# Kernel tuning notes

Measured on AMD Instinct MI355X. Metric: run time of the kernel, lower is better.

The kernel has to match this reference:

```python
import jax, jax.numpy as jnp
import numpy as np

BINS = 100
ALPHA = 0.1

def entropy_batch(h):
    # Faithful to torch: histogram path is detached (done in numpy in original).
    h = jax.lax.stop_gradient(h)
    B, D = h.shape
    hp = h - jnp.min(h, axis=1, keepdims=True)
    hn = hp / jnp.max(hp, axis=1, keepdims=True)  # normalized to [0, 1]
    # np.histogram with `bins` uniform bins over [0,1]; rightmost edge inclusive -> clip
    idx = jnp.clip(jnp.floor(hn * BINS).astype(jnp.int32), 0, BINS - 1)
    rows = jnp.arange(B)[:, None]
    counts = jnp.zeros((B, BINS), jnp.float32).at[rows, idx].add(1.0)
    px = counts / jnp.float32(D)
    safe = jnp.where(px > 0, px, 1.0)
    ent = -jnp.sum(px * jnp.log(safe), axis=1) + jnp.log(jnp.float32(BINS))
    return jnp.mean(ent)

def setup_inputs() -> dict:
    key = jax.random.key(0)
    ks = jax.random.split(key, 8)
    B = 65536
    archi = [246, 246, 246, 246, 246, 246]
    dims = [784] + archi
    inp = {"x": jax.random.normal(ks[0], (B, 1, 28, 28), jnp.float32)}
    for i in range(6):
        inp[f"W{i+1}"] = 0.01 * jax.random.normal(ks[i + 1], (dims[i + 1], dims[i]), jnp.float32)
        inp[f"b{i+1}"] = jnp.zeros((dims[i + 1],), jnp.float32)
    inp["W7"] = 0.01 * jax.random.normal(ks[7], (10, archi[-1]), jnp.float32)
    inp["b7"] = jnp.zeros((10,), jnp.float32)
    return inp

def reference(x, W1, b1, W2, b2, W3, b3, W4, b4, W5, b5, W6, b6, W7, b7):
    h = x.reshape(-1, 784)
    Hs = []
    for W, b in ((W1, b1), (W2, b2), (W3, b3), (W4, b4), (W5, b5), (W6, b6)):
        h = jax.nn.leaky_relu(h @ W.T + b, negative_slope=ALPHA)
        Hs.append(entropy_batch(h))
    logits = jax.nn.relu(h @ W7.T + b7)
    out = jax.nn.log_softmax(logits, axis=1)
    return (out, Hs[0], Hs[1], Hs[2], Hs[3], Hs[4], Hs[5])
```

## Files before the change

kernel.cpp:

```cpp
#include <hip/hip_runtime.h>
#include <cstdint>
#include <cmath>

#define BATCH 65536
#define NREAL 246
#define NPAD  256
#define K1    784
#define K1PAD 832
#define BINS  100
#define ALPHA 0.1f
#define RB    32
#define NBLK  (BATCH/RB)

typedef __bf16 bf16x8 __attribute__((ext_vector_type(8)));
typedef __bf16 bf16x4 __attribute__((ext_vector_type(4)));
typedef float  f32x4  __attribute__((ext_vector_type(4)));

#define OFF_HS     0
#define OFF_STAGE  16384
#define OFF_HIST   16384
#define OFF_MN     29184
#define OFF_MX     29696
#define OFF_WENT   30208
#define LDS_TOTAL  30336

__global__ __launch_bounds__(256)
void pad_weights(const float* __restrict__ W1, const float* __restrict__ W2,
                 const float* __restrict__ W3, const float* __restrict__ W4,
                 const float* __restrict__ W5, const float* __restrict__ W6,
                 const float* __restrict__ W7,
                 const float* __restrict__ b1, const float* __restrict__ b2,
                 const float* __restrict__ b3, const float* __restrict__ b4,
                 const float* __restrict__ b5, const float* __restrict__ b6,
                 __bf16* __restrict__ W1p, __bf16* __restrict__ Wp,
                 __bf16* __restrict__ W7p, float* __restrict__ bpad)
{
    int tid = blockIdx.x * 256 + threadIdx.x;
    const int n1 = NPAD * K1PAD;
    const int n2 = 5 * NPAD * NPAD;
    const int n3 = 16 * NPAD;
    if (tid < n1) {
        int row = tid / K1PAD;
        int k   = tid - row * K1PAD;
        W1p[tid] = (__bf16)((row < NREAL && k < K1) ? W1[row * K1 + k] : 0.0f);
    } else if (tid < n1 + n2) {
        int t = tid - n1;
        int wsel = t >> 16;
        int idx  = t & 65535;
        int row  = idx >> 8, k = idx & 255;
        const float* W = (wsel == 0) ? W2 : (wsel == 1) ? W3 : (wsel == 2) ? W4
                        : (wsel == 3) ? W5 : W6;
        Wp[t] = (__bf16)((row < NREAL && k < NREAL) ? W[row * NREAL + k] : 0.0f);
    } else if (tid < n1 + n2 + n3) {
        int t = tid - n1 - n2;
        int row = t >> 8, k = t & 255;
        W7p[t] = (__bf16)((row < 10 && k < NREAL) ? W7[row * NREAL + k] : 0.0f);
    } else if (tid < n1 + n2 + n3 + 6 * NPAD) {
        int t = tid - n1 - n2 - n3;
        int li = t >> 8, k = t & 255;
        const float* b = (li == 0) ? b1 : (li == 1) ? b2 : (li == 2) ? b3
                        : (li == 3) ? b4 : (li == 4) ? b5 : b6;
        bpad[t] = (k < NREAL) ? b[k] : 0.0f;
    }
}

__global__ __launch_bounds__(256)
void mega(const float* __restrict__ x,
          const __bf16* __restrict__ W1p,
          const __bf16* __restrict__ Wp,
          const __bf16* __restrict__ W7p,
          const float* __restrict__ bpad,
          const float* __restrict__ b7,
          float* __restrict__ out, float* __restrict__ partial)
{
    __shared__ char smem[LDS_TOTAL];
    char*  Hb    = smem + OFF_HS;
    float* rowmn = (float*)(smem + OFF_MN);
    float* rowmx = (float*)(smem + OFF_MX);
    float* went  = (float*)(smem + OFF_WENT);
    int*   hist  = (int*)(smem + OFF_HIST);

    const int tid = threadIdx.x;
    const int w = tid >> 6, l = tid & 63;
    const int lane16 = l & 15, lane4 = l >> 4;
    const int m0 = blockIdx.x * RB;

    const int rg = l >> 3, q = l & 7;
    const int erow = w * 8 + rg;
    const int eswz = (erow & 7) << 4;
    int* histW = hist + w * 800;

    f32x4 acc[2][4];
#pragma unroll
    for (int i = 0; i < 2; ++i)
#pragma unroll
        for (int j = 0; j < 4; ++j) acc[i][j] = f32x4{0.f, 0.f, 0.f, 0.f};

    bf16x8 Bq[2][4];

    auto loadBq = [&](int s, const __bf16* Bbase, int hh) {
        const __bf16* pp = Bbase + (size_t)(w * 64 + lane16) * NPAD + (hh >> 1) * 64 + (hh & 1) * 32 + lane4 * 8;
#pragma unroll
        for (int j = 0; j < 4; ++j)
            Bq[s][j] = *(const bf16x8*)(pp + (size_t)j * 16 * NPAD);
    };

    auto epilogue = [&](const float* bp) {
        f32x4 bq[4];
#pragma unroll
        for (int j = 0; j < 4; ++j)
            bq[j] = *(const f32x4*)(bp + w * 64 + j * 16 + lane4 * 4);
#pragma unroll
        for (int i = 0; i < 2; ++i) {
            const int m = i * 16 + lane16;
            const int swz = (m & 7) << 4;
            float mn = 1e30f, mx = -1e30f;
#pragma unroll
            for (int j = 0; j < 4; ++j) {
                const int nbase = w * 64 + j * 16 + lane4 * 4;
                bf16x4 hv;
#pragma unroll
                for (int r = 0; r < 4; ++r) {
                    float v = acc[i][j][r] + bq[j][r];
                    v = v > 0.0f ? v : ALPHA * v;
                    bool valid = (nbase + r) < NREAL;
                    hv[r] = valid ? (__bf16)v : (__bf16)0.0f;
                    float vb = (float)hv[r];
                    mn = fminf(mn, valid ? vb : 1e30f);
                    mx = fmaxf(mx, valid ? vb : -1e30f);
                }
                *(bf16x4*)(Hb + m * 512 + ((nbase * 2) ^ swz)) = hv;
            }
            mn = fminf(mn, __shfl_xor(mn, 16, 64));
            mx = fmaxf(mx, __shfl_xor(mx, 16, 64));
            mn = fminf(mn, __shfl_xor(mn, 32, 64));
            mx = fmaxf(mx, __shfl_xor(mx, 32, 64));
            if (lane4 == 0) { rowmn[m * 4 + w] = mn; rowmx[m * 4 + w] = mx; }
        }
    };

    auto esum = [&](int li) {
        const int* hrow = histW + rg * 100;
        float S = 0.0f;
#pragma unroll
        for (int t = 0; t < 13; ++t) {
            int b = q * 13 + t;
            if (b < 100) {
                float f = (float)hrow[b];
                float g = fmaxf(f, 1.0f);
                S = fmaf(f, __logf(g), S);
            }
        }
#pragma unroll
        for (int off = 1; off < 64; off <<= 1) S += __shfl_xor(S, off, 64);
        if (l == 0) went[w * 6 + li] = 8.0f * logf(246.0f) - S * (1.0f / 246.0f);
    };

    {
        const int srow = tid >> 3;
        const int skc  = (tid & 7) * 8;
        float4 xr0, xr1;
        auto issueX = [&](int kt) {
            int k0 = kt * 64 + skc;
            if (k0 < K1) {
                const float* gx = x + (size_t)(m0 + srow) * K1 + k0;
                xr0 = *(const float4*)gx;
                xr1 = *(const float4*)(gx + 4);
            } else {
                xr0 = float4{0.f,0.f,0.f,0.f};
                xr1 = float4{0.f,0.f,0.f,0.f};
            }
        };
        auto writeX = [&](int buf) {
            bf16x8 h;
            h[0]=(__bf16)xr0.x; h[1]=(__bf16)xr0.y; h[2]=(__bf16)xr0.z; h[3]=(__bf16)xr0.w;
            h[4]=(__bf16)xr1.x; h[5]=(__bf16)xr1.y; h[6]=(__bf16)xr1.z; h[7]=(__bf16)xr1.w;
            char* st = smem + OFF_STAGE + buf * 4096;
            *(bf16x8*)(st + srow * 128 + ((skc * 2) ^ ((srow & 7) << 4))) = h;
        };
        auto lB = [&](int s, int kt, int kk) {
            const __bf16* p = W1p + (size_t)(w * 64 + lane16) * K1PAD + kt * 64 + kk * 32 + lane4 * 8;
#pragma unroll
            for (int j = 0; j < 4; ++j)
                Bq[s][j] = *(const bf16x8*)(p + (size_t)j * 16 * K1PAD);
        };
        auto cH = [&](const char* st, int kbyte, int s) {
#pragma unroll
            for (int i = 0; i < 2; ++i) {
                int m = i * 16 + lane16;
                bf16x8 af = *(const bf16x8*)(st + m * 128 + ((kbyte + lane4 * 16) ^ ((m & 7) << 4)));
                __builtin_amdgcn_s_setprio(1);
#pragma unroll
                for (int j = 0; j < 4; ++j)
                    acc[i][j] = __builtin_amdgcn_mfma_f32_16x16x32_bf16(s ? Bq[1][j] : Bq[0][j], af, acc[i][j], 0, 0, 0);
                __builtin_amdgcn_s_setprio(0);
            }
        };

        issueX(0); writeX(0); issueX(1);
        lB(0, 0, 0);
        for (int kt = 0; kt < 13; ++kt) {
            __syncthreads();
            if (kt < 12) { writeX((kt + 1) & 1); if (kt < 11) issueX(kt + 2); }
            const char* st = smem + OFF_STAGE + (kt & 1) * 4096;
            lB(1, kt, 1);
            cH(st, 0, 0);
            if (kt < 12) lB(0, kt + 1, 0);
            cH(st, 64, 1);
        }
    }

    loadBq(0, Wp, 0);
    loadBq(1, Wp, 1);
    epilogue(bpad);
    __syncthreads();

    for (int p = 0; p < 5; ++p) {
        const __bf16* WpP = Wp + (size_t)p * (NPAD * NPAD);
        const __bf16* WpN = WpP + NPAD * NPAD;

#pragma unroll
        for (int i = 0; i < 2; ++i)
#pragma unroll
            for (int j = 0; j < 4; ++j) acc[i][j] = f32x4{0.f, 0.f, 0.f, 0.f};

#pragma unroll
        for (int t = 0; t < 13; ++t) { int b = t * 64 + l; if (b < 800) histW[b] = 0; }
        f32x4 m4 = *(const f32x4*)(rowmn + erow * 4);
        f32x4 x4 = *(const f32x4*)(rowmx + erow * 4);
        float emn = fminf(fminf(m4[0], m4[1]), fminf(m4[2], m4[3]));
        float emx = fmaxf(fmaxf(x4[0], x4[1]), fmaxf(x4[2], x4[3]));
        float ers = (emx > emn) ? 100.0f / (emx - emn) : 0.0f;
        float eb  = -emn * ers;
        asm volatile("s_waitcnt lgkmcnt(0)" ::: "memory");

#pragma unroll
        for (int h = 0; h < 8; ++h) {
#pragma unroll
            for (int i = 0; i < 2; ++i) {
                int m = i * 16 + lane16;
                bf16x8 af = *(const bf16x8*)(Hb + m * 512 + ((h * 64 + lane4 * 16) ^ ((m & 7) << 4)));
                __builtin_amdgcn_s_setprio(1);
#pragma unroll
                for (int j = 0; j < 4; ++j)
                    acc[i][j] = __builtin_amdgcn_mfma_f32_16x16x32_bf16((h & 1) ? Bq[1][j] : Bq[0][j],
                                                                        af, acc[i][j], 0, 0, 0);
                __builtin_amdgcn_s_setprio(0);
            }
            if (h < 6)      loadBq(h & 1, WpP, h + 2);
            else if (p < 4) loadBq(h & 1, WpN, h - 6);
            {
                int c0 = q * 32 + h * 4;
                bf16x4 hv = *(const bf16x4*)(Hb + erow * 512 + ((c0 * 2) ^ eswz));
#pragma unroll
                for (int e = 0; e < 4; ++e) {
                    if (c0 + e < NREAL) {
                        int idx = (int)fmaf((float)hv[e], ers, eb);
                        idx = idx > BINS - 1 ? BINS - 1 : (idx < 0 ? 0 : idx);
                        atomicAdd(&histW[rg * 100 + idx], 1);
                    }
                }
            }
        }
        asm volatile("s_waitcnt lgkmcnt(0)" ::: "memory");
        esum(p);

        __syncthreads();
        epilogue(bpad + (size_t)(p + 1) * NPAD);
        __syncthreads();
    }

    {
#pragma unroll
        for (int t = 0; t < 13; ++t) { int b = t * 64 + l; if (b < 800) histW[b] = 0; }
        f32x4 m4 = *(const f32x4*)(rowmn + erow * 4);
        f32x4 x4 = *(const f32x4*)(rowmx + erow * 4);
        float emn = fminf(fminf(m4[0], m4[1]), fminf(m4[2], m4[3]));
        float emx = fmaxf(fmaxf(x4[0], x4[1]), fmaxf(x4[2], x4[3]));
        float ers = (emx > emn) ? 100.0f / (emx - emn) : 0.0f;
        float eb  = -emn * ers;
        asm volatile("s_waitcnt lgkmcnt(0)" ::: "memory");
#pragma unroll
        for (int h = 0; h < 8; ++h) {
            int c0 = q * 32 + h * 4;
            bf16x4 hv = *(const bf16x4*)(Hb + erow * 512 + ((c0 * 2) ^ eswz));
#pragma unroll
            for (int e = 0; e < 4; ++e) {
                if (c0 + e < NREAL) {
                    int idx = (int)fmaf((float)hv[e], ers, eb);
                    idx = idx > BINS - 1 ? BINS - 1 : (idx < 0 ? 0 : idx);
                    atomicAdd(&histW[rg * 100 + idx], 1);
                }
            }
        }
        asm volatile("s_waitcnt lgkmcnt(0)" ::: "memory");
        esum(5);
    }

    if (w < 2) {
        f32x4 hacc = f32x4{0.f, 0.f, 0.f, 0.f};
        int row = w * 16 + lane16;
#pragma unroll
        for (int kt = 0; kt < 8; ++kt) {
            bf16x8 af = *(const bf16x8*)(Hb + row * 512 + ((kt * 64 + lane4 * 16) ^ ((row & 7) << 4)));
            bf16x8 bf = *(const bf16x8*)(W7p + (size_t)lane16 * NPAD + kt * 32 + lane4 * 8);
            hacc = __builtin_amdgcn_mfma_f32_16x16x32_bf16(af, bf, hacc, 0, 0, 0);
        }
        float bv = (lane16 < 10) ? b7[lane16] : 0.0f;
#pragma unroll
        for (int r = 0; r < 4; ++r) {
            float lg = fmaxf(hacc[r] + bv, 0.0f);
            float vm = (lane16 < 10) ? lg : -1e30f;
#pragma unroll
            for (int off = 8; off; off >>= 1) vm = fmaxf(vm, __shfl_xor(vm, off, 64));
            float ex = (lane16 < 10) ? expf(lg - vm) : 0.0f;
#pragma unroll
            for (int off = 8; off; off >>= 1) ex += __shfl_xor(ex, off, 64);
            float ls = vm + logf(ex);
            if (lane16 < 10) {
                int grow = m0 + w * 16 + lane4 * 4 + r;
                out[(size_t)grow * 10 + lane16] = lg - ls;
            }
        }
    }

    __syncthreads();
    if (tid < 6) {
        float s = went[tid] + went[6 + tid] + went[12 + tid] + went[18 + tid];
        partial[tid * NBLK + blockIdx.x] = s;
    }
}

__global__ __launch_bounds__(256)
void reduce_kernel(const float* __restrict__ partial, float* __restrict__ out)
{
    __shared__ float s[256];
    const int li = blockIdx.x, tid = threadIdx.x;
    float a = 0.0f;
    for (int i = tid; i < NBLK; i += 256) a += partial[li * NBLK + i];
    s[tid] = a;
    __syncthreads();
    for (int st = 128; st; st >>= 1) {
        if (tid < st) s[tid] += s[tid + st];
        __syncthreads();
    }
    if (tid == 0)
        out[(size_t)BATCH * 10 + li] = s[0] / (float)BATCH + logf((float)BINS);
}

extern "C" void kernel_launch(void* const* d_in, const int* in_sizes, int n_in,
                              void* d_out, int out_size, void* d_ws, size_t ws_size,
                              hipStream_t stream)
{
    (void)in_sizes; (void)n_in; (void)out_size; (void)ws_size;

    const float* x  = (const float*)d_in[0];
    const float* W1 = (const float*)d_in[1];
    const float* b1 = (const float*)d_in[2];
    const float* W2 = (const float*)d_in[3];
    const float* b2 = (const float*)d_in[4];
    const float* W3 = (const float*)d_in[5];
    const float* b3 = (const float*)d_in[6];
    const float* W4 = (const float*)d_in[7];
    const float* b4 = (const float*)d_in[8];
    const float* W5 = (const float*)d_in[9];
    const float* b5 = (const float*)d_in[10];
    const float* W6 = (const float*)d_in[11];
    const float* b6 = (const float*)d_in[12];
    const float* W7 = (const float*)d_in[13];
    const float* b7 = (const float*)d_in[14];

    char* ws = (char*)d_ws;
    __bf16* W1p = (__bf16*)(ws);
    __bf16* Wp  = (__bf16*)(ws + 425984);
    __bf16* W7p = (__bf16*)(ws + 1081344);
    float*  bpad = (float*)(ws + 1089536);
    float*  partial = (float*)(ws + 1095680);
    float*  out = (float*)d_out;

    pad_weights<<<2134, 256, 0, stream>>>(W1, W2, W3, W4, W5, W6, W7,
                                          b1, b2, b3, b4, b5, b6,
                                          W1p, Wp, W7p, bpad);
    mega<<<NBLK, 256, 0, stream>>>(x, W1p, Wp, W7p, bpad, b7, out, partial);
    reduce_kernel<<<6, 256, 0, stream>>>(partial, out);
}
```

Measured before the change: 293.1 us.

## Use 8 waves per block with 32-column slices per wave in mega kernel

Doubles the block from 256 to 512 threads so each of 8 waves computes a 32-column slice of the 32-row tile instead of 64 columns. The X staging, histogram rows per wave, min/max partials and the per-wave entropy bookkeeping are all reworked for the new split. The aim is more latency hiding and parallel work per block, at the cost of halving the MFMA work per wave, duplicating A-fragment LDS reads across more waves, and adding more per-wave reductions.

```diff
diff --git a/kernel.cpp b/kernel.cpp
--- a/kernel.cpp
+++ b/kernel.cpp
@@ -14,15 +14,16 @@
 
 typedef __bf16 bf16x8 __attribute__((ext_vector_type(8)));
 typedef __bf16 bf16x4 __attribute__((ext_vector_type(4)));
+typedef __bf16 bf16x2 __attribute__((ext_vector_type(2)));
 typedef float  f32x4  __attribute__((ext_vector_type(4)));
 
 #define OFF_HS     0
 #define OFF_STAGE  16384
 #define OFF_HIST   16384
 #define OFF_MN     29184
-#define OFF_MX     29696
-#define OFF_WENT   30208
-#define LDS_TOTAL  30336
+#define OFF_MX     30208
+#define OFF_WENT   31232
+#define LDS_TOTAL  31424
 
 __global__ __launch_bounds__(256)
 void pad_weights(const float* __restrict__ W1, const float* __restrict__ W2,
@@ -64,7 +65,7 @@
     }
 }
 
-__global__ __launch_bounds__(256)
+__global__ __launch_bounds__(512)
 void mega(const float* __restrict__ x,
           const __bf16* __restrict__ W1p,
           const __bf16* __restrict__ Wp,
@@ -83,41 +84,42 @@
     const int tid = threadIdx.x;
     const int w = tid >> 6, l = tid & 63;
     const int lane16 = l & 15, lane4 = l >> 4;
+    const int wc = w * 32;
     const int m0 = blockIdx.x * RB;
 
-    const int rg = l >> 3, q = l & 7;
-    const int erow = w * 8 + rg;
+    const int rg = l >> 4, q = l & 15;
+    const int erow = w * 4 + rg;
     const int eswz = (erow & 7) << 4;
-    int* histW = hist + w * 800;
-
-    f32x4 acc[2][4];
+    int* histW = hist + w * 400;
+
+    f32x4 acc[2][2];
 #pragma unroll
     for (int i = 0; i < 2; ++i)
 #pragma unroll
-        for (int j = 0; j < 4; ++j) acc[i][j] = f32x4{0.f, 0.f, 0.f, 0.f};
-
-    bf16x8 Bq[2][4];
+        for (int j = 0; j < 2; ++j) acc[i][j] = f32x4{0.f, 0.f, 0.f, 0.f};
+
+    bf16x8 Bq[2][2];
 
     auto loadBq = [&](int s, const __bf16* Bbase, int hh) {
-        const __bf16* pp = Bbase + (size_t)(w * 64 + lane16) * NPAD + (hh >> 1) * 64 + (hh & 1) * 32 + lane4 * 8;
-#pragma unroll
-        for (int j = 0; j < 4; ++j)
+        const __bf16* pp = Bbase + (size_t)(wc + lane16) * NPAD + hh * 32 + lane4 * 8;
+#pragma unroll
+        for (int j = 0; j < 2; ++j)
             Bq[s][j] = *(const bf16x8*)(pp + (size_t)j * 16 * NPAD);
     };
 
     auto epilogue = [&](const float* bp) {
-        f32x4 bq[4];
-#pragma unroll
-        for (int j = 0; j < 4; ++j)
-            bq[j] = *(const f32x4*)(bp + w * 64 + j * 16 + lane4 * 4);
+        f32x4 bq[2];
+#pragma unroll
+        for (int j = 0; j < 2; ++j)
+            bq[j] = *(const f32x4*)(bp + wc + j * 16 + lane4 * 4);
 #pragma unroll
         for (int i = 0; i < 2; ++i) {
             const int m = i * 16 + lane16;
             const int swz = (m & 7) << 4;
             float mn = 1e30f, mx = -1e30f;
 #pragma unroll
-            for (int j = 0; j < 4; ++j) {
-                const int nbase = w * 64 + j * 16 + lane4 * 4;
+            for (int j = 0; j < 2; ++j) {
+                const int nbase = wc + j * 16 + lane4 * 4;
                 bf16x4 hv;
 #pragma unroll
                 for (int r = 0; r < 4; ++r) {
@@ -135,7 +137,7 @@
             mx = fmaxf(mx, __shfl_xor(mx, 16, 64));
             mn = fminf(mn, __shfl_xor(mn, 32, 64));
             mx = fmaxf(mx, __shfl_xor(mx, 32, 64));
-            if (lane4 == 0) { rowmn[m * 4 + w] = mn; rowmx[m * 4 + w] = mx; }
+            if (lane4 == 0) { rowmn[m * 8 + w] = mn; rowmx[m * 8 + w] = mx; }
         }
     };
 
@@ -143,8 +145,8 @@
         const int* hrow = histW + rg * 100;
         float S = 0.0f;
 #pragma unroll
-        for (int t = 0; t < 13; ++t) {
-            int b = q * 13 + t;
+        for (int t = 0; t < 7; ++t) {
+            int b = q * 7 + t;
             if (b < 100) {
                 float f = (float)hrow[b];
                 float g = fmaxf(f, 1.0f);
@@ -153,35 +155,31 @@
         }
 #pragma unroll
         for (int off = 1; off < 64; off <<= 1) S += __shfl_xor(S, off, 64);
-        if (l == 0) went[w * 6 + li] = 8.0f * logf(246.0f) - S * (1.0f / 246.0f);
+        if (l == 0) went[w * 6 + li] = 4.0f * logf(246.0f) - S * (1.0f / 246.0f);
     };
 
     {
-        const int srow = tid >> 3;
-        const int skc  = (tid & 7) * 8;
-        float4 xr0, xr1;
+        const int srow = tid >> 4;
+        const int skc  = (tid & 15) * 4;
+        float4 xr;
         auto issueX = [&](int kt) {
             int k0 = kt * 64 + skc;
             if (k0 < K1) {
-                const float* gx = x + (size_t)(m0 + srow) * K1 + k0;
-                xr0 = *(const float4*)gx;
-                xr1 = *(const float4*)(gx + 4);
+                xr = *(const float4*)(x + (size_t)(m0 + srow) * K1 + k0);
             } else {
-                xr0 = float4{0.f,0.f,0.f,0.f};
-                xr1 = float4{0.f,0.f,0.f,0.f};
+                xr = float4{0.f, 0.f, 0.f, 0.f};
             }
         };
         auto writeX = [&](int buf) {
-            bf16x8 h;
-            h[0]=(__bf16)xr0.x; h[1]=(__bf16)xr0.y; h[2]=(__bf16)xr0.z; h[3]=(__bf16)xr0.w;
-            h[4]=(__bf16)xr1.x; h[5]=(__bf16)xr1.y; h[6]=(__bf16)xr1.z; h[7]=(__bf16)xr1.w;
+            bf16x4 h;
+            h[0]=(__bf16)xr.x; h[1]=(__bf16)xr.y; h[2]=(__bf16)xr.z; h[3]=(__bf16)xr.w;
             char* st = smem + OFF_STAGE + buf * 4096;
-            *(bf16x8*)(st + srow * 128 + ((skc * 2) ^ ((srow & 7) << 4))) = h;
+            *(bf16x4*)(st + srow * 128 + ((skc * 2) ^ ((srow & 7) << 4))) = h;
         };
         auto lB = [&](int s, int kt, int kk) {
-            const __bf16* p = W1p + (size_t)(w * 64 + lane16) * K1PAD + kt * 64 + kk * 32 + lane4 * 8;
-#pragma unroll
-            for (int j = 0; j < 4; ++j)
+            const __bf16* p = W1p + (size_t)(wc + lane16) * K1PAD + kt * 64 + kk * 32 + lane4 * 8;
+#pragma unroll
+            for (int j = 0; j < 2; ++j)
                 Bq[s][j] = *(const bf16x8*)(p + (size_t)j * 16 * K1PAD);
         };
         auto cH = [&](const char* st, int kbyte, int s) {
@@ -191,7 +189,7 @@
                 bf16x8 af = *(const bf16x8*)(st + m * 128 + ((kbyte + lane4 * 16) ^ ((m & 7) << 4)));
                 __builtin_amdgcn_s_setprio(1);
 #pragma unroll
-                for (int j = 0; j < 4; ++j)
+                for (int j = 0; j < 2; ++j)
                     acc[i][j] = __builtin_amdgcn_mfma_f32_16x16x32_bf16(s ? Bq[1][j] : Bq[0][j], af, acc[i][j], 0, 0, 0);
                 __builtin_amdgcn_s_setprio(0);
             }
@@ -222,14 +220,18 @@
 #pragma unroll
         for (int i = 0; i < 2; ++i)
 #pragma unroll
-            for (int j = 0; j < 4; ++j) acc[i][j] = f32x4{0.f, 0.f, 0.f, 0.f};
-
-#pragma unroll
-        for (int t = 0; t < 13; ++t) { int b = t * 64 + l; if (b < 800) histW[b] = 0; }
-        f32x4 m4 = *(const f32x4*)(rowmn + erow * 4);
-        f32x4 x4 = *(const f32x4*)(rowmx + erow * 4);
-        float emn = fminf(fminf(m4[0], m4[1]), fminf(m4[2], m4[3]));
-        float emx = fmaxf(fmaxf(x4[0], x4[1]), fmaxf(x4[2], x4[3]));
+            for (int j = 0; j < 2; ++j) acc[i][j] = f32x4{0.f, 0.f, 0.f, 0.f};
+
+#pragma unroll
+        for (int t = 0; t < 7; ++t) { int b = t * 64 + l; if (b < 400) histW[b] = 0; }
+        f32x4 m4 = *(const f32x4*)(rowmn + erow * 8);
+        f32x4 m5 = *(const f32x4*)(rowmn + erow * 8 + 4);
+        f32x4 x4 = *(const f32x4*)(rowmx + erow * 8);
+        f32x4 x5 = *(const f32x4*)(rowmx + erow * 8 + 4);
+        float emn = fminf(fminf(fminf(m4[0], m4[1]), fminf(m4[2], m4[3])),
+                          fminf(fminf(m5[0], m5[1]), fminf(m5[2], m5[3])));
+        float emx = fmaxf(fmaxf(fmaxf(x4[0], x4[1]), fmaxf(x4[2], x4[3])),
+                          fmaxf(fmaxf(x5[0], x5[1]), fmaxf(x5[2], x5[3])));
         float ers = (emx > emn) ? 100.0f / (emx - emn) : 0.0f;
         float eb  = -emn * ers;
         asm volatile("s_waitcnt lgkmcnt(0)" ::: "memory");
@@ -242,7 +244,7 @@
                 bf16x8 af = *(const bf16x8*)(Hb + m * 512 + ((h * 64 + lane4 * 16) ^ ((m & 7) << 4)));
                 __builtin_amdgcn_s_setprio(1);
 #pragma unroll
-                for (int j = 0; j < 4; ++j)
+                for (int j = 0; j < 2; ++j)
                     acc[i][j] = __builtin_amdgcn_mfma_f32_16x16x32_bf16((h & 1) ? Bq[1][j] : Bq[0][j],
                                                                         af, acc[i][j], 0, 0, 0);
                 __builtin_amdgcn_s_setprio(0);
@@ -250,10 +252,10 @@
             if (h < 6)      loadBq(h & 1, WpP, h + 2);
             else if (p < 4) loadBq(h & 1, WpN, h - 6);
             {
-                int c0 = q * 32 + h * 4;
-                bf16x4 hv = *(const bf16x4*)(Hb + erow * 512 + ((c0 * 2) ^ eswz));
-#pragma unroll
-                for (int e = 0; e < 4; ++e) {
+                int c0 = q * 16 + h * 2;
+                bf16x2 hv = *(const bf16x2*)(Hb + erow * 512 + ((c0 * 2) ^ eswz));
+#pragma unroll
+                for (int e = 0; e < 2; ++e) {
                     if (c0 + e < NREAL) {
                         int idx = (int)fmaf((float)hv[e], ers, eb);
                         idx = idx > BINS - 1 ? BINS - 1 : (idx < 0 ? 0 : idx);
@@ -272,20 +274,24 @@
 
     {
 #pragma unroll
-        for (int t = 0; t < 13; ++t) { int b = t * 64 + l; if (b < 800) histW[b] = 0; }
-        f32x4 m4 = *(const f32x4*)(rowmn + erow * 4);
-        f32x4 x4 = *(const f32x4*)(rowmx + erow * 4);
-        float emn = fminf(fminf(m4[0], m4[1]), fminf(m4[2], m4[3]));
-        float emx = fmaxf(fmaxf(x4[0], x4[1]), fmaxf(x4[2], x4[3]));
+        for (int t = 0; t < 7; ++t) { int b = t * 64 + l; if (b < 400) histW[b] = 0; }
+        f32x4 m4 = *(const f32x4*)(rowmn + erow * 8);
+        f32x4 m5 = *(const f32x4*)(rowmn + erow * 8 + 4);
+        f32x4 x4 = *(const f32x4*)(rowmx + erow * 8);
+        f32x4 x5 = *(const f32x4*)(rowmx + erow * 8 + 4);
+        float emn = fminf(fminf(fminf(m4[0], m4[1]), fminf(m4[2], m4[3])),
+                          fminf(fminf(m5[0], m5[1]), fminf(m5[2], m5[3])));
+        float emx = fmaxf(fmaxf(fmaxf(x4[0], x4[1]), fmaxf(x4[2], x4[3])),
+                          fmaxf(fmaxf(x5[0], x5[1]), fmaxf(x5[2], x5[3])));
         float ers = (emx > emn) ? 100.0f / (emx - emn) : 0.0f;
         float eb  = -emn * ers;
         asm volatile("s_waitcnt lgkmcnt(0)" ::: "memory");
 #pragma unroll
         for (int h = 0; h < 8; ++h) {
-            int c0 = q * 32 + h * 4;
-            bf16x4 hv = *(const bf16x4*)(Hb + erow * 512 + ((c0 * 2) ^ eswz));
-#pragma unroll
-            for (int e = 0; e < 4; ++e) {
+            int c0 = q * 16 + h * 2;
+            bf16x2 hv = *(const bf16x2*)(Hb + erow * 512 + ((c0 * 2) ^ eswz));
+#pragma unroll
+            for (int e = 0; e < 2; ++e) {
                 if (c0 + e < NREAL) {
                     int idx = (int)fmaf((float)hv[e], ers, eb);
                     idx = idx > BINS - 1 ? BINS - 1 : (idx < 0 ? 0 : idx);
@@ -326,7 +332,9 @@
 
     __syncthreads();
     if (tid < 6) {
-        float s = went[tid] + went[6 + tid] + went[12 + tid] + went[18 + tid];
+        float s = 0.0f;
+#pragma unroll
+        for (int qq = 0; qq < 8; ++qq) s += went[qq * 6 + tid];
         partial[tid * NBLK + blockIdx.x] = s;
     }
 }
@@ -381,6 +389,6 @@
     pad_weights<<<2134, 256, 0, stream>>>(W1, W2, W3, W4, W5, W6, W7,
                                           b1, b2, b3, b4, b5, b6,
                                           W1p, Wp, W7p, bpad);
-    mega<<<NBLK, 256, 0, stream>>>(x, W1p, Wp, W7p, bpad, b7, out, partial);
+    mega<<<NBLK, 512, 0, stream>>>(x, W1p, Wp, W7p, bpad, b7, out, partial);
     reduce_kernel<<<6, 256, 0, stream>>>(partial, out);
 }
```

After: 290.4 us. Within noise of the previous version (-1.0%).
